# Performance work log

Measured on AMD Instinct MI355X. Metric: run time of the kernel, lower is better.

Reference implementation:

```python
import jax, jax.numpy as jnp
import numpy as np

B, L, F, P, E, H, D, C, V = 256, 100, 8, 4, 64, 4, 64, 32, 10000
HD = H * D  # 256 = att_dim * head_num
TOWER_IN = F * E + F * E + P * E + C  # 1312
LN_EPS = 1e-3  # keras LayerNormalization default epsilon


def _ln(x, g, b):
    m = jnp.mean(x, axis=-1, keepdims=True)
    v = jnp.mean(jnp.square(x - m), axis=-1, keepdims=True)
    return (x - m) * jax.lax.rsqrt(v + LN_EPS) * g + b


def setup_inputs() -> dict:
    key = jax.random.key(0)
    ks = jax.random.split(key, 32)
    w = lambda k, s: jax.random.normal(k, s, jnp.float32) * 0.02
    inp = {
        'target_ad': jax.random.randint(ks[0], (B, F), 0, V),
        'ubs_feature': jax.random.randint(ks[1], (B, L, F), 0, V),
        'profile_feature': jax.random.randint(ks[2], (B, P), 0, V),
        'context_feature': jax.random.normal(ks[3], (B, C), jnp.float32),
        # embedding tables: one per sparse feature, stacked
        'item_tables': w(ks[4], (F, V, E)),
        'profile_tables': w(ks[5], (P, V, E)),
        # per-timestep distinct attention weights, stacked over L
        'q_w': w(ks[6], (L, E, HD)),
        'k_w': w(ks[7], (L, E, HD)),
        'v_w': w(ks[8], (L, E, HD)),
        'lin_w': w(ks[9], (L, HD, E)),
        'lin_b': jnp.zeros((L, E), jnp.float32),
        # shared post-attention layernorm
        'ln_g': jnp.ones((E,), jnp.float32),
        'ln_b': jnp.zeros((E,), jnp.float32),
        # dense tower
        't_w1': w(ks[10], (TOWER_IN, 1024)), 't_b1': jnp.zeros((1024,), jnp.float32),
        't_g1': jnp.ones((1024,), jnp.float32), 't_bb1': jnp.zeros((1024,), jnp.float32),
        't_w2': w(ks[11], (1024, 512)), 't_b2': jnp.zeros((512,), jnp.float32),
        't_g2': jnp.ones((512,), jnp.float32), 't_bb2': jnp.zeros((512,), jnp.float32),
        't_w3': w(ks[12], (512, 256)), 't_b3': jnp.zeros((256,), jnp.float32),
        't_g3': jnp.ones((256,), jnp.float32), 't_bb3': jnp.zeros((256,), jnp.float32),
        't_w4': w(ks[13], (256, 1)), 't_b4': jnp.zeros((1,), jnp.float32),
    }
    return inp


def reference(target_ad, ubs_feature, profile_feature, context_feature,
              item_tables, profile_tables, q_w, k_w, v_w, lin_w, lin_b,
              ln_g, ln_b,
              t_w1, t_b1, t_g1, t_bb1,
              t_w2, t_b2, t_g2, t_bb2,
              t_w3, t_b3, t_g3, t_bb3,
              t_w4, t_b4):
    b = target_ad.shape[0]
    # embedding lookups (feature-wise tables)
    te = item_tables[jnp.arange(F)[None, :], target_ad]              # [B,F,E]
    ue = item_tables[jnp.arange(F)[None, None, :], ubs_feature]      # [B,L,F,E]
    pe = profile_tables[jnp.arange(P)[None, :], profile_feature]     # [B,P,E]

    # per-step distinct Q/K/V projections, batched over L via einsum
    q = jnp.einsum('blfe,leo->blfo', ue, q_w).reshape(b, L, F, H, D)
    k = jnp.einsum('blfe,leo->blfo', ue, k_w).reshape(b, L, F, H, D)
    v = jnp.einsum('blfe,leo->blfo', ue, v_w).reshape(b, L, F, H, D)
    scores = jnp.einsum('blfhd,blghd->blhfg', q, k) / jnp.sqrt(jnp.float32(D))
    attw = jax.nn.softmax(scores, axis=-1)                           # [B,L,H,F,F]
    att = jnp.einsum('blhfg,blghd->blfhd', attw, v).reshape(b, L, F, HD)
    att_out = jnp.einsum('blfo,loe->blfe', att, lin_w) + lin_b[None, :, None, :]
    # shared LayerNorm per step, summed over L (original accumulates into zeros_like)
    ubs_t = jnp.sum(_ln(att_out, ln_g, ln_b), axis=1)                # [B,F,E]
    ubs = jax.nn.relu(ubs_t / jnp.float32(L))

    total = jnp.concatenate([ubs.reshape(b, -1), te.reshape(b, -1),
                             pe.reshape(b, -1), context_feature], axis=-1)

    h = jax.nn.relu(_ln(total @ t_w1 + t_b1, t_g1, t_bb1))
    h = jax.nn.relu(_ln(h @ t_w2 + t_b2, t_g2, t_bb2))
    h = jax.nn.relu(_ln(h @ t_w3 + t_b3, t_g3, t_bb3))
    out = jax.nn.sigmoid(h @ t_w4 + t_b4)                            # [B,1]
    return out
```

## Files before the change

kernel.cpp:

```cpp
#include <hip/hip_runtime.h>
#include <hip/hip_bf16.h>

#define B_ 256
#define L_ 100
#define F_ 8
#define P_ 4
#define E_ 64
#define H_ 4
#define D_ 64
#define C_ 32
#define V_ 10000
#define TOWER_IN_ 1312
#define LN_EPS 0.001f
#define LCH_ 4
#define NCH_ 25
#define ZK_ 40

typedef __attribute__((ext_vector_type(8))) short bf8v;
typedef __attribute__((ext_vector_type(8))) unsigned short us8;
typedef __attribute__((ext_vector_type(4))) float f4v;

__device__ __forceinline__ unsigned short f2bf(float x) {
    __hip_bfloat16 h = __float2bfloat16(x);
    return __builtin_bit_cast(unsigned short, h);
}

#define BARRIER() do { \
    asm volatile("s_waitcnt lgkmcnt(0)" ::: "memory"); \
    __builtin_amdgcn_s_barrier(); \
    asm volatile("" ::: "memory"); \
} while (0)

__global__ __launch_bounds__(256) void prologue_kernel(
    const float* __restrict__ q_w, const float* __restrict__ k_w,
    const float* __restrict__ v_w, const float* __restrict__ lin_w,
    unsigned short* __restrict__ wsMT, unsigned short* __restrict__ wsWT,
    const float* __restrict__ w1, const float* __restrict__ w2,
    const float* __restrict__ w3,
    unsigned short* __restrict__ Wt1, unsigned short* __restrict__ Wt2,
    unsigned short* __restrict__ Wt3, float* __restrict__ ubs_acc)
{
    __shared__ float sA[64][68];
    __shared__ float sB[64][68];
    const int t = threadIdx.x;
    const int bx = blockIdx.x;

    if (bx < 400) {
        const int l = bx >> 2;
        const int h = bx & 3;
        const size_t obase = (size_t)(l * 4 + h) * 4096;
        const int te = t & 15, to = t >> 4;

        for (int i = 0; i < 16; ++i) {
            int idx = t + i * 256;
            int e = idx >> 6, d = idx & 63;
            sA[e][d] = q_w[(l * 64 + e) * 256 + h * 64 + d];
            sB[e][d] = k_w[(l * 64 + e) * 256 + h * 64 + d];
        }
        __syncthreads();
        {
            float acc[4][4];
            #pragma unroll
            for (int i = 0; i < 4; ++i)
                #pragma unroll
                for (int j = 0; j < 4; ++j) acc[i][j] = 0.f;
            for (int d0 = 0; d0 < 64; d0 += 4) {
                float4 a4[4], b4[4];
                #pragma unroll
                for (int i = 0; i < 4; ++i) a4[i] = *(const float4*)&sA[te + 16 * i][d0];
                #pragma unroll
                for (int j = 0; j < 4; ++j) b4[j] = *(const float4*)&sB[to + 16 * j][d0];
                #pragma unroll
                for (int i = 0; i < 4; ++i)
                    #pragma unroll
                    for (int j = 0; j < 4; ++j) {
                        acc[i][j] += a4[i].x * b4[j].x;
                        acc[i][j] += a4[i].y * b4[j].y;
                        acc[i][j] += a4[i].z * b4[j].z;
                        acc[i][j] += a4[i].w * b4[j].w;
                    }
            }
            #pragma unroll
            for (int j = 0; j < 4; ++j)
                #pragma unroll
                for (int i = 0; i < 4; ++i)
                    wsMT[obase + (to + 16 * j) * 64 + (te + 16 * i)] = f2bf(acc[i][j]);
        }
        __syncthreads();

        for (int i = 0; i < 16; ++i) {
            int idx = t + i * 256;
            int e = idx >> 6, d = idx & 63;
            sA[e][d] = v_w[(l * 64 + e) * 256 + h * 64 + d];
            int oo = idx & 63, dd = idx >> 6;
            sB[oo][dd] = lin_w[l * 16384 + (h * 64 + dd) * 64 + oo];
        }
        __syncthreads();
        {
            float acc[4][4];
            #pragma unroll
            for (int i = 0; i < 4; ++i)
                #pragma unroll
                for (int j = 0; j < 4; ++j) acc[i][j] = 0.f;
            for (int d0 = 0; d0 < 64; d0 += 4) {
                float4 a4[4], b4[4];
                #pragma unroll
                for (int i = 0; i < 4; ++i) a4[i] = *(const float4*)&sA[te + 16 * i][d0];
                #pragma unroll
                for (int j = 0; j < 4; ++j) b4[j] = *(const float4*)&sB[to + 16 * j][d0];
                #pragma unroll
                for (int i = 0; i < 4; ++i)
                    #pragma unroll
                    for (int j = 0; j < 4; ++j) {
                        acc[i][j] += a4[i].x * b4[j].x;
                        acc[i][j] += a4[i].y * b4[j].y;
                        acc[i][j] += a4[i].z * b4[j].z;
                        acc[i][j] += a4[i].w * b4[j].w;
                    }
            }
            #pragma unroll
            for (int j = 0; j < 4; ++j)
                #pragma unroll
                for (int i = 0; i < 4; ++i)
                    wsWT[obase + (to + 16 * j) * 64 + (te + 16 * i)] = f2bf(acc[i][j]);
        }
    } else if (bx < 2352) {
        float (*tile)[33] = (float (*)[33])sA;
        int bi = bx - 400;
        const float* src; unsigned short* dst; int K, N, tk, tn;
        if (bi < 1312)      { src = w1; dst = Wt1; K = 1312; N = 1024; tk = bi / 32;  tn = bi % 32; }
        else if (bi < 1824) { int i = bi - 1312; src = w2; dst = Wt2; K = 1024; N = 512; tk = i / 16; tn = i % 16; }
        else                { int i = bi - 1824; src = w3; dst = Wt3; K = 512;  N = 256; tk = i / 8;  tn = i % 8; }
        const int k0 = tk * 32, n0 = tn * 32;
        const int rr = t >> 5, cc = t & 31;
        #pragma unroll
        for (int i = 0; i < 4; ++i) {
            int r = rr * 4 + i;
            tile[r][cc] = src[(size_t)(k0 + r) * N + n0 + cc];
        }
        __syncthreads();
        #pragma unroll
        for (int i = 0; i < 4; ++i) {
            int r = rr * 4 + i;
            dst[(size_t)(n0 + r) * K + k0 + cc] = f2bf(tile[cc][r]);
        }
    } else {
        const int bi = bx - 2352;
        float4 z = {0.f, 0.f, 0.f, 0.f};
        *(float4*)(ubs_acc + (size_t)bi * 1024 + t * 4) = z;
    }
}

__global__ __launch_bounds__(256, 3) void attn_kernel(
    const int* __restrict__ ubs_feature, const float* __restrict__ item_tables,
    const unsigned short* __restrict__ wsMT, const unsigned short* __restrict__ wsWT,
    const float* __restrict__ lin_b, const float* __restrict__ ln_g,
    const float* __restrict__ ln_b, float* __restrict__ ubs_acc)
{
    __shared__ __align__(16) unsigned short sUE[64][72];
    __shared__ __align__(16) unsigned short sT[64][136];
    __shared__ __align__(16) unsigned short sZt[4][64][ZK_];
    __shared__ __align__(16) unsigned short sAblk[4][16][32];
    __shared__ float sLng[64], sLnb[64], sLinb[LCH_][64];

    const int t = threadIdx.x;
    const int c = blockIdx.x >> 5;
    const int b0 = (blockIdx.x & 31) * 8;
    const int wv = t >> 6, lane = t & 63, quad = lane >> 4, cl = lane & 15;
    const int role = wv >> 1, hlw = wv & 1;

    const int grow = wv * 16 + (lane >> 2);
    const int gseg = lane & 3;
    const int gb = b0 + (grow >> 3), gf = grow & 7;

    if (t < 64) { sLng[t] = ln_g[t]; sLnb[t] = ln_b[t]; }
    if (t >= 64 && t < 128) {
        #pragma unroll
        for (int li = 0; li < LCH_; ++li)
            sLinb[li][t - 64] = lin_b[(c * LCH_ + li) * 64 + (t - 64)];
    }

    int vidx[LCH_];
    #pragma unroll
    for (int li = 0; li < LCH_; ++li)
        vidx[li] = ubs_feature[(gb * L_ + c * LCH_ + li) * F_ + gf];

    float4 pf[4];
    bf8v bfrag[4][2];

    auto load_bfrag = [&](int lh) {
        const unsigned short* Bsrc = (role == 0 ? wsMT : wsWT) + ((size_t)lh * 4096);
        #pragma unroll
        for (int nt = 0; nt < 4; ++nt)
            #pragma unroll
            for (int k2 = 0; k2 < 2; ++k2)
                bfrag[nt][k2] = *(const bf8v*)(Bsrc + (nt * 16 + cl) * 64 + k2 * 32 + quad * 8);
    };
    auto load_pf = [&](int li) {
        const float* srcp = item_tables + ((size_t)gf * V_ + vidx[li]) * 64 + gseg * 16;
        #pragma unroll
        for (int j = 0; j < 4; ++j) pf[j] = ((const float4*)srcp)[j];
    };
    auto store_ue = [&]() {
        us8 u0, u1;
        u0[0] = f2bf(pf[0].x); u0[1] = f2bf(pf[0].y); u0[2] = f2bf(pf[0].z); u0[3] = f2bf(pf[0].w);
        u0[4] = f2bf(pf[1].x); u0[5] = f2bf(pf[1].y); u0[6] = f2bf(pf[1].z); u0[7] = f2bf(pf[1].w);
        u1[0] = f2bf(pf[2].x); u1[1] = f2bf(pf[2].y); u1[2] = f2bf(pf[2].z); u1[3] = f2bf(pf[2].w);
        u1[4] = f2bf(pf[3].x); u1[5] = f2bf(pf[3].y); u1[6] = f2bf(pf[3].z); u1[7] = f2bf(pf[3].w);
        *(us8*)&sUE[grow][gseg * 16]     = u0;
        *(us8*)&sUE[grow][gseg * 16 + 8] = u1;
    };

    load_pf(0);
    load_bfrag((c * LCH_) * 4 + hlw);
    store_ue();
    BARRIER();

    float lnacc[16];
    #pragma unroll
    for (int i = 0; i < 16; ++i) lnacc[i] = 0.f;

    for (int li = 0; li < LCH_; ++li) {
        const int l = c * LCH_ + li;

        if (li + 1 < LCH_) load_pf(li + 1);

        f4v accO[4];
        #pragma unroll
        for (int nt = 0; nt < 4; ++nt) accO[nt] = {0.f, 0.f, 0.f, 0.f};

        #pragma unroll
        for (int half = 0; half < 2; ++half) {
            #pragma unroll
            for (int m = 0; m < 4; ++m) {
                bf8v a0 = *(const bf8v*)&sUE[m * 16 + cl][quad * 8];
                bf8v a1 = *(const bf8v*)&sUE[m * 16 + cl][32 + quad * 8];
                #pragma unroll
                for (int nt = 0; nt < 4; ++nt) {
                    f4v acc = {0.f, 0.f, 0.f, 0.f};
                    acc = __builtin_amdgcn_mfma_f32_16x16x32_bf16(a0, bfrag[nt][0], acc, 0, 0, 0);
                    acc = __builtin_amdgcn_mfma_f32_16x16x32_bf16(a1, bfrag[nt][1], acc, 0, 0, 0);
                    if (role == 0) {
                        #pragma unroll
                        for (int j = 0; j < 4; ++j)
                            sT[m * 16 + quad * 4 + j][hlw * 64 + nt * 16 + cl] = f2bf(acc[j]);
                    } else {
                        ushort4 zp;
                        zp.x = f2bf(acc[0]); zp.y = f2bf(acc[1]);
                        zp.z = f2bf(acc[2]); zp.w = f2bf(acc[3]);
                        const int k0 = (quad >> 1) * 16 + hlw * 8 + (quad & 1) * 4;
                        *(ushort4*)&sZt[m][nt * 16 + cl][k0] = zp;
                    }
                }
            }
            if (half == 0)            load_bfrag(l * 4 + 2 + hlw);
            else if (li + 1 < LCH_)   load_bfrag((l + 1) * 4 + hlw);
            BARRIER();

            {
                const int p = wv;
                const bool valid = (cl >> 3) == (quad >> 1);
                #pragma unroll
                for (int hl = 0; hl < 2; ++hl) {
                    bf8v a0s = *(const bf8v*)&sT[p * 16 + cl][hl * 64 + quad * 8];
                    bf8v a1s = *(const bf8v*)&sT[p * 16 + cl][hl * 64 + 32 + quad * 8];
                    bf8v u0 = *(const bf8v*)&sUE[p * 16 + cl][quad * 8];
                    bf8v u1 = *(const bf8v*)&sUE[p * 16 + cl][32 + quad * 8];
                    f4v acc = {0.f, 0.f, 0.f, 0.f};
                    acc = __builtin_amdgcn_mfma_f32_16x16x32_bf16(a0s, u0, acc, 0, 0, 0);
                    acc = __builtin_amdgcn_mfma_f32_16x16x32_bf16(a1s, u1, acc, 0, 0, 0);
                    const int kk = hl * 8 + (cl & 7) + (cl >> 3) * 16;
                    #pragma unroll
                    for (int j = 0; j < 4; ++j) {
                        float v = acc[j] * 0.125f;
                        float mx = v;
                        mx = fmaxf(mx, __shfl_xor(mx, 1));
                        mx = fmaxf(mx, __shfl_xor(mx, 2));
                        mx = fmaxf(mx, __shfl_xor(mx, 4));
                        float ex = __expf(v - mx);
                        float sm = ex;
                        sm += __shfl_xor(sm, 1);
                        sm += __shfl_xor(sm, 2);
                        sm += __shfl_xor(sm, 4);
                        float aw = valid ? ex * __builtin_amdgcn_rcpf(sm) : 0.f;
                        sAblk[p][quad * 4 + j][kk] = f2bf(aw);
                    }
                }
            }

            {
                const int p = wv;
                bf8v a0p = *(const bf8v*)&sAblk[p][cl][quad * 8];
                #pragma unroll
                for (int nt = 0; nt < 4; ++nt) {
                    bf8v bz = *(const bf8v*)&sZt[p][nt * 16 + cl][quad * 8];
                    accO[nt] = __builtin_amdgcn_mfma_f32_16x16x32_bf16(a0p, bz, accO[nt], 0, 0, 0);
                }
            }
            BARRIER();
        }

        {
            float x[16];
            #pragma unroll
            for (int nt = 0; nt < 4; ++nt)
                #pragma unroll
                for (int j = 0; j < 4; ++j)
                    x[nt * 4 + j] = accO[nt][j] + sLinb[li][nt * 16 + cl];
            #pragma unroll
            for (int j = 0; j < 4; ++j) {
                float s = x[j] + x[4 + j] + x[8 + j] + x[12 + j];
                #pragma unroll
                for (int m = 1; m < 16; m <<= 1) s += __shfl_xor(s, m);
                float mean = s * (1.f / 64.f);
                float q = 0.f;
                #pragma unroll
                for (int nt = 0; nt < 4; ++nt) { float d = x[nt * 4 + j] - mean; q += d * d; }
                #pragma unroll
                for (int m = 1; m < 16; m <<= 1) q += __shfl_xor(q, m);
                float rst = rsqrtf(q * (1.f / 64.f) + LN_EPS);
                #pragma unroll
                for (int nt = 0; nt < 4; ++nt) {
                    int col = nt * 16 + cl;
                    lnacc[nt * 4 + j] += (x[nt * 4 + j] - mean) * rst * sLng[col] + sLnb[col];
                }
            }
        }

        if (li + 1 < LCH_) {
            store_ue();
            BARRIER();
        }
    }

    #pragma unroll
    for (int j = 0; j < 4; ++j) {
        const int row = wv * 16 + quad * 4 + j;
        const int b = b0 + (row >> 3), f = row & 7;
        #pragma unroll
        for (int nt = 0; nt < 4; ++nt)
            atomicAdd(&ubs_acc[(size_t)b * 512 + f * 64 + nt * 16 + cl], lnacc[nt * 4 + j]);
    }
}

__global__ __launch_bounds__(256) void reduceX_kernel(
    const float* __restrict__ ubs_acc,
    const int* __restrict__ target_ad, const int* __restrict__ profile_feature,
    const float* __restrict__ context,
    const float* __restrict__ item_tables, const float* __restrict__ profile_tables,
    unsigned short* __restrict__ X, float* __restrict__ statsAll)
{
    const int b = blockIdx.x, t = threadIdx.x;
    if (b == B_) {
        float4 z = {0.f, 0.f, 0.f, 0.f};
        ((float4*)statsAll)[t] = z;
        return;
    }
    const float2 v = *(const float2*)(ubs_acc + (size_t)b * 512 + t * 2);
    X[b * TOWER_IN_ + t * 2]     = f2bf(fmaxf(v.x * 0.01f, 0.f));
    X[b * TOWER_IN_ + t * 2 + 1] = f2bf(fmaxf(v.y * 0.01f, 0.f));
    for (int cc = 512 + t; cc < TOWER_IN_; cc += 256) {
        float x;
        if (cc < 1024) { int j = cc - 512, f = j >> 6, e = j & 63;
            x = item_tables[((size_t)f * V_ + target_ad[b * 8 + f]) * 64 + e]; }
        else if (cc < 1280) { int j = cc - 1024, pp = j >> 6, e = j & 63;
            x = profile_tables[((size_t)pp * V_ + profile_feature[b * 4 + pp]) * 64 + e]; }
        else x = context[b * 32 + (cc - 1280)];
        X[b * TOWER_IN_ + cc] = f2bf(x);
    }
}

__global__ __launch_bounds__(256) void gemm_kernel(
    const unsigned short* __restrict__ A, const unsigned short* __restrict__ Bw,
    const float* __restrict__ bias, float* __restrict__ C, int K, int N,
    float* __restrict__ stats)
{
    const int t = threadIdx.x;
    const int wv = t >> 6, lane = t & 63, quad = lane >> 4, cl = lane & 15;
    const int n0 = blockIdx.x * 64 + wv * 16;
    const int m0 = blockIdx.y * 16;
    f4v acc0 = {0.f, 0.f, 0.f, 0.f};
    f4v acc1 = {0.f, 0.f, 0.f, 0.f};
    const unsigned short* arow = A + (size_t)(m0 + cl) * K + quad * 8;
    const unsigned short* brow = Bw + (size_t)(n0 + cl) * K + quad * 8;
    int k0 = 0;
    #pragma unroll 2
    for (; k0 + 64 <= K; k0 += 64) {
        bf8v a0 = *(const bf8v*)(arow + k0);
        bf8v b0 = *(const bf8v*)(brow + k0);
        bf8v a1 = *(const bf8v*)(arow + k0 + 32);
        bf8v b1 = *(const bf8v*)(brow + k0 + 32);
        acc0 = __builtin_amdgcn_mfma_f32_16x16x32_bf16(a0, b0, acc0, 0, 0, 0);
        acc1 = __builtin_amdgcn_mfma_f32_16x16x32_bf16(a1, b1, acc1, 0, 0, 0);
    }
    if (k0 < K) {
        bf8v a = *(const bf8v*)(arow + k0);
        bf8v b = *(const bf8v*)(brow + k0);
        acc0 = __builtin_amdgcn_mfma_f32_16x16x32_bf16(a, b, acc0, 0, 0, 0);
    }
    float bv = bias[n0 + cl];
    float cj[4];
    #pragma unroll
    for (int j = 0; j < 4; ++j) {
        cj[j] = acc0[j] + acc1[j] + bv;
        C[(size_t)(m0 + quad * 4 + j) * N + n0 + cl] = cj[j];
    }
    if (stats) {
        #pragma unroll
        for (int j = 0; j < 4; ++j) {
            float s = cj[j], q = cj[j] * cj[j];
            #pragma unroll
            for (int m = 1; m < 16; m <<= 1) { s += __shfl_xor(s, m); q += __shfl_xor(q, m); }
            if (cl == 0) {
                const int row = m0 + quad * 4 + j;
                atomicAdd(&stats[row * 2], s);
                atomicAdd(&stats[row * 2 + 1], q);
            }
        }
    }
}

__global__ __launch_bounds__(256) void lnapply_kernel(
    const float* __restrict__ C, const float* __restrict__ stats,
    const float* __restrict__ g, const float* __restrict__ bb,
    unsigned short* __restrict__ Hx, int N, float invN)
{
    const int b = blockIdx.x, t = threadIdx.x;
    const float s = stats[b * 2], q = stats[b * 2 + 1];
    const float mean = s * invN;
    const float var  = q * invN - mean * mean;
    const float rst  = rsqrtf(fmaxf(var, 0.f) + LN_EPS);
    for (int j = t * 4; j < N; j += 1024) {
        float4 x = *(const float4*)(C + (size_t)b * N + j);
        ushort4 o;
        o.x = f2bf(fmaxf((x.x - mean) * rst * g[j]     + bb[j],     0.f));
        o.y = f2bf(fmaxf((x.y - mean) * rst * g[j + 1] + bb[j + 1], 0.f));
        o.z = f2bf(fmaxf((x.z - mean) * rst * g[j + 2] + bb[j + 2], 0.f));
        o.w = f2bf(fmaxf((x.w - mean) * rst * g[j + 3] + bb[j + 3], 0.f));
        *(ushort4*)(Hx + (size_t)b * N + j) = o;
    }
}

__device__ __forceinline__ float block_reduce_sum(float v, float* sRed) {
    #pragma unroll
    for (int m = 1; m < 64; m <<= 1) v += __shfl_xor(v, m, 64);
    int wave = threadIdx.x >> 6, lane = threadIdx.x & 63;
    __syncthreads();
    if (lane == 0) sRed[wave] = v;
    __syncthreads();
    return sRed[0] + sRed[1] + sRed[2] + sRed[3];
}

__global__ __launch_bounds__(256) void final_kernel(
    const float* __restrict__ C3, const float* __restrict__ g3,
    const float* __restrict__ bb3, const float* __restrict__ w4,
    const float* __restrict__ b4, float* __restrict__ out)
{
    __shared__ float sRed[4];
    const int b = blockIdx.x, t = threadIdx.x;
    float x = C3[b * 256 + t];
    float s = block_reduce_sum(x, sRed);
    float mean = s * (1.f / 256.f);
    float d = x - mean;
    __syncthreads();
    float q = block_reduce_sum(d * d, sRed);
    float rst = rsqrtf(q * (1.f / 256.f) + LN_EPS);
    float h = fmaxf(d * rst * g3[t] + bb3[t], 0.f);
    __syncthreads();
    float p = block_reduce_sum(h * w4[t], sRed);
    if (t == 0) out[b] = 1.f / (1.f + expf(-(p + b4[0])));
}

extern "C" void kernel_launch(void* const* d_in, const int* in_sizes, int n_in,
                              void* d_out, int out_size, void* d_ws, size_t ws_size,
                              hipStream_t stream)
{
    (void)in_sizes; (void)n_in; (void)out_size; (void)ws_size;
    const int*   target_ad       = (const int*)d_in[0];
    const int*   ubs_feature     = (const int*)d_in[1];
    const int*   profile_feature = (const int*)d_in[2];
    const float* context         = (const float*)d_in[3];
    const float* item_tables     = (const float*)d_in[4];
    const float* profile_tables  = (const float*)d_in[5];
    const float* q_w   = (const float*)d_in[6];
    const float* k_w   = (const float*)d_in[7];
    const float* v_w   = (const float*)d_in[8];
    const float* lin_w = (const float*)d_in[9];
    const float* lin_b = (const float*)d_in[10];
    const float* ln_g  = (const float*)d_in[11];
    const float* ln_b  = (const float*)d_in[12];
    const float* t_w1  = (const float*)d_in[13];
    const float* t_b1  = (const float*)d_in[14];
    const float* t_g1  = (const float*)d_in[15];
    const float* t_bb1 = (const float*)d_in[16];
    const float* t_w2  = (const float*)d_in[17];
    const float* t_b2  = (const float*)d_in[18];
    const float* t_g2  = (const float*)d_in[19];
    const float* t_bb2 = (const float*)d_in[20];
    const float* t_w3  = (const float*)d_in[21];
    const float* t_b3  = (const float*)d_in[22];
    const float* t_g3  = (const float*)d_in[23];
    const float* t_bb3 = (const float*)d_in[24];
    const float* t_w4  = (const float*)d_in[25];
    const float* t_b4  = (const float*)d_in[26];

    char* ws = (char*)d_ws;
    unsigned short* wsMT = (unsigned short*)(ws);
    unsigned short* wsWT = (unsigned short*)(ws +  3276800);
    float* ubs_acc       = (float*)         (ws +  6553600);
    unsigned short* Wt1  = (unsigned short*)(ws +  7077888);
    unsigned short* Wt2  = (unsigned short*)(ws +  9764864);
    unsigned short* Wt3  = (unsigned short*)(ws + 10813440);
    unsigned short* X    = (unsigned short*)(ws + 11075584);
    float*          C1   = (float*)         (ws + 11747328);
    unsigned short* H1   = (unsigned short*)(ws + 12795904);
    float*          C2   = (float*)         (ws + 13320192);
    unsigned short* H2   = (unsigned short*)(ws + 13844480);
    float*          C3   = (float*)         (ws + 14106624);
    float* stats1        = (float*)(ws);
    float* stats2        = (float*)(ws + 2048);

    prologue_kernel<<<2480, 256, 0, stream>>>(q_w, k_w, v_w, lin_w, wsMT, wsWT,
                                              t_w1, t_w2, t_w3, Wt1, Wt2, Wt3, ubs_acc);
    attn_kernel<<<NCH_ * 32, 256, 0, stream>>>(ubs_feature, item_tables, wsMT, wsWT,
                                               lin_b, ln_g, ln_b, ubs_acc);
    reduceX_kernel<<<B_ + 1, 256, 0, stream>>>(ubs_acc, target_ad, profile_feature, context,
                                               item_tables, profile_tables, X, stats1);
    gemm_kernel<<<dim3(16, 16), 256, 0, stream>>>(X,  Wt1, t_b1, C1, 1312, 1024, stats1);
    lnapply_kernel<<<B_, 256, 0, stream>>>(C1, stats1, t_g1, t_bb1, H1, 1024, 1.f / 1024.f);
    gemm_kernel<<<dim3(8, 16),  256, 0, stream>>>(H1, Wt2, t_b2, C2, 1024, 512, stats2);
    lnapply_kernel<<<B_, 256, 0, stream>>>(C2, stats2, t_g2, t_bb2, H2, 512, 1.f / 512.f);
    gemm_kernel<<<dim3(4, 16),  256, 0, stream>>>(H2, Wt3, t_b3, C3, 512, 256, (float*)nullptr);
    final_kernel<<<B_, 256, 0, stream>>>(C3, t_g3, t_bb3, t_w4, t_b4, (float*)d_out);
}
```

Measured before the change: 265.6 us.

## Fuse tower stages into fewer kernels and overlap weight transpose with attention

The tower weight transposes move from the prologue into the attention kernel launch as extra blocks, so they can run alongside attention work. The X-building step is fused into the first GEMM, and each LayerNorm+ReLU is fused into the next GEMM's A-tile load into LDS. The third GEMM is fused with the final LayerNorm, dot product and sigmoid. Together this cuts the launch count from nine to five and removes the intermediate X/H buffers and stats atomics, at the cost of recomputing per-row LN stats in every column block and using a smaller grid for the last GEMM.

Result: faster. 257.5 us (median of 2 runs) (-3.1%).

```diff
diff --git a/kernel.cpp b/kernel.cpp
--- a/kernel.cpp
+++ b/kernel.cpp
@@ -31,102 +31,125 @@
     asm volatile("" ::: "memory"); \
 } while (0)
 
-__global__ __launch_bounds__(256) void prologue_kernel(
+__global__ __launch_bounds__(256) void pre_kernel(
     const float* __restrict__ q_w, const float* __restrict__ k_w,
     const float* __restrict__ v_w, const float* __restrict__ lin_w,
     unsigned short* __restrict__ wsMT, unsigned short* __restrict__ wsWT,
-    const float* __restrict__ w1, const float* __restrict__ w2,
-    const float* __restrict__ w3,
-    unsigned short* __restrict__ Wt1, unsigned short* __restrict__ Wt2,
-    unsigned short* __restrict__ Wt3, float* __restrict__ ubs_acc)
+    float* __restrict__ ubs_acc)
 {
     __shared__ float sA[64][68];
     __shared__ float sB[64][68];
     const int t = threadIdx.x;
     const int bx = blockIdx.x;
 
-    if (bx < 400) {
-        const int l = bx >> 2;
-        const int h = bx & 3;
-        const size_t obase = (size_t)(l * 4 + h) * 4096;
-        const int te = t & 15, to = t >> 4;
-
-        for (int i = 0; i < 16; ++i) {
-            int idx = t + i * 256;
-            int e = idx >> 6, d = idx & 63;
-            sA[e][d] = q_w[(l * 64 + e) * 256 + h * 64 + d];
-            sB[e][d] = k_w[(l * 64 + e) * 256 + h * 64 + d];
-        }
-        __syncthreads();
-        {
-            float acc[4][4];
+    if (bx >= 400) {
+        const int bi = bx - 400;
+        float4 z = {0.f, 0.f, 0.f, 0.f};
+        *(float4*)(ubs_acc + (size_t)bi * 1024 + t * 4) = z;
+        return;
+    }
+
+    const int l = bx >> 2;
+    const int h = bx & 3;
+    const size_t obase = (size_t)(l * 4 + h) * 4096;
+    const int te = t & 15, to = t >> 4;
+
+    for (int i = 0; i < 16; ++i) {
+        int idx = t + i * 256;
+        int e = idx >> 6, d = idx & 63;
+        sA[e][d] = q_w[(l * 64 + e) * 256 + h * 64 + d];
+        sB[e][d] = k_w[(l * 64 + e) * 256 + h * 64 + d];
+    }
+    __syncthreads();
+    {
+        float acc[4][4];
+        #pragma unroll
+        for (int i = 0; i < 4; ++i)
+            #pragma unroll
+            for (int j = 0; j < 4; ++j) acc[i][j] = 0.f;
+        for (int d0 = 0; d0 < 64; d0 += 4) {
+            float4 a4[4], b4[4];
+            #pragma unroll
+            for (int i = 0; i < 4; ++i) a4[i] = *(const float4*)&sA[te + 16 * i][d0];
+            #pragma unroll
+            for (int j = 0; j < 4; ++j) b4[j] = *(const float4*)&sB[to + 16 * j][d0];
             #pragma unroll
             for (int i = 0; i < 4; ++i)
                 #pragma unroll
-                for (int j = 0; j < 4; ++j) acc[i][j] = 0.f;
-            for (int d0 = 0; d0 < 64; d0 += 4) {
-                float4 a4[4], b4[4];
-                #pragma unroll
-                for (int i = 0; i < 4; ++i) a4[i] = *(const float4*)&sA[te + 16 * i][d0];
-                #pragma unroll
-                for (int j = 0; j < 4; ++j) b4[j] = *(const float4*)&sB[to + 16 * j][d0];
-                #pragma unroll
-                for (int i = 0; i < 4; ++i)
-                    #pragma unroll
-                    for (int j = 0; j < 4; ++j) {
-                        acc[i][j] += a4[i].x * b4[j].x;
-                        acc[i][j] += a4[i].y * b4[j].y;
-                        acc[i][j] += a4[i].z * b4[j].z;
-                        acc[i][j] += a4[i].w * b4[j].w;
-                    }
-            }
-            #pragma unroll
-            for (int j = 0; j < 4; ++j)
-                #pragma unroll
-                for (int i = 0; i < 4; ++i)
-                    wsMT[obase + (to + 16 * j) * 64 + (te + 16 * i)] = f2bf(acc[i][j]);
-        }
-        __syncthreads();
-
-        for (int i = 0; i < 16; ++i) {
-            int idx = t + i * 256;
-            int e = idx >> 6, d = idx & 63;
-            sA[e][d] = v_w[(l * 64 + e) * 256 + h * 64 + d];
-            int oo = idx & 63, dd = idx >> 6;
-            sB[oo][dd] = lin_w[l * 16384 + (h * 64 + dd) * 64 + oo];
-        }
-        __syncthreads();
-        {
-            float acc[4][4];
+                for (int j = 0; j < 4; ++j) {
+                    acc[i][j] += a4[i].x * b4[j].x;
+                    acc[i][j] += a4[i].y * b4[j].y;
+                    acc[i][j] += a4[i].z * b4[j].z;
+                    acc[i][j] += a4[i].w * b4[j].w;
+                }
+        }
+        #pragma unroll
+        for (int j = 0; j < 4; ++j)
             #pragma unroll
             for (int i = 0; i < 4; ++i)
-                #pragma unroll
-                for (int j = 0; j < 4; ++j) acc[i][j] = 0.f;
-            for (int d0 = 0; d0 < 64; d0 += 4) {
-                float4 a4[4], b4[4];
-                #pragma unroll
-                for (int i = 0; i < 4; ++i) a4[i] = *(const float4*)&sA[te + 16 * i][d0];
-                #pragma unroll
-                for (int j = 0; j < 4; ++j) b4[j] = *(const float4*)&sB[to + 16 * j][d0];
-                #pragma unroll
-                for (int i = 0; i < 4; ++i)
-                    #pragma unroll
-                    for (int j = 0; j < 4; ++j) {
-                        acc[i][j] += a4[i].x * b4[j].x;
-                        acc[i][j] += a4[i].y * b4[j].y;
-                        acc[i][j] += a4[i].z * b4[j].z;
-                        acc[i][j] += a4[i].w * b4[j].w;
-                    }
-            }
-            #pragma unroll
-            for (int j = 0; j < 4; ++j)
-                #pragma unroll
-                for (int i = 0; i < 4; ++i)
-                    wsWT[obase + (to + 16 * j) * 64 + (te + 16 * i)] = f2bf(acc[i][j]);
-        }
-    } else if (bx < 2352) {
-        float (*tile)[33] = (float (*)[33])sA;
-        int bi = bx - 400;
+                wsMT[obase + (to + 16 * j) * 64 + (te + 16 * i)] = f2bf(acc[i][j]);
+    }
+    __syncthreads();
+
+    for (int i = 0; i < 16; ++i) {
+        int idx = t + i * 256;
+        int e = idx >> 6, d = idx & 63;
+        sA[e][d] = v_w[(l * 64 + e) * 256 + h * 64 + d];
+        int oo = idx & 63, dd = idx >> 6;
+        sB[oo][dd] = lin_w[l * 16384 + (h * 64 + dd) * 64 + oo];
+    }
+    __syncthreads();
+    {
+        float acc[4][4];
+        #pragma unroll
+        for (int i = 0; i < 4; ++i)
+            #pragma unroll
+            for (int j = 0; j < 4; ++j) acc[i][j] = 0.f;
+        for (int d0 = 0; d0 < 64; d0 += 4) {
+            float4 a4[4], b4[4];
+            #pragma unroll
+            for (int i = 0; i < 4; ++i) a4[i] = *(const float4*)&sA[te + 16 * i][d0];
+            #pragma unroll
+            for (int j = 0; j < 4; ++j) b4[j] = *(const float4*)&sB[to + 16 * j][d0];
+            #pragma unroll
+            for (int i = 0; i < 4; ++i)
+                #pragma unroll
+                for (int j = 0; j < 4; ++j) {
+                    acc[i][j] += a4[i].x * b4[j].x;
+                    acc[i][j] += a4[i].y * b4[j].y;
+                    acc[i][j] += a4[i].z * b4[j].z;
+                    acc[i][j] += a4[i].w * b4[j].w;
+                }
+        }
+        #pragma unroll
+        for (int j = 0; j < 4; ++j)
+            #pragma unroll
+            for (int i = 0; i < 4; ++i)
+                wsWT[obase + (to + 16 * j) * 64 + (te + 16 * i)] = f2bf(acc[i][j]);
+    }
+}
+
+__global__ __launch_bounds__(256, 3) void attn_kernel(
+    const int* __restrict__ ubs_feature, const float* __restrict__ item_tables,
+    const unsigned short* __restrict__ wsMT, const unsigned short* __restrict__ wsWT,
+    const float* __restrict__ lin_b, const float* __restrict__ ln_g,
+    const float* __restrict__ ln_b, float* __restrict__ ubs_acc,
+    const float* __restrict__ w1, const float* __restrict__ w2,
+    const float* __restrict__ w3,
+    unsigned short* __restrict__ Wt1, unsigned short* __restrict__ Wt2,
+    unsigned short* __restrict__ Wt3)
+{
+    __shared__ __align__(16) unsigned short sUE[64][72];
+    __shared__ __align__(16) unsigned short sT[64][136];
+    __shared__ __align__(16) unsigned short sZt[4][64][ZK_];
+    __shared__ __align__(16) unsigned short sAblk[4][16][32];
+    __shared__ float sLng[64], sLnb[64], sLinb[LCH_][64];
+
+    const int t = threadIdx.x;
+
+    if (blockIdx.x >= 800) {
+        float (*tile)[33] = (float (*)[33])sT;
+        int bi = blockIdx.x - 800;
         const float* src; unsigned short* dst; int K, N, tk, tn;
         if (bi < 1312)      { src = w1; dst = Wt1; K = 1312; N = 1024; tk = bi / 32;  tn = bi % 32; }
         else if (bi < 1824) { int i = bi - 1312; src = w2; dst = Wt2; K = 1024; N = 512; tk = i / 16; tn = i % 16; }
@@ -144,26 +167,9 @@
             int r = rr * 4 + i;
             dst[(size_t)(n0 + r) * K + k0 + cc] = f2bf(tile[cc][r]);
         }
-    } else {
-        const int bi = bx - 2352;
-        float4 z = {0.f, 0.f, 0.f, 0.f};
-        *(float4*)(ubs_acc + (size_t)bi * 1024 + t * 4) = z;
-    }
-}
-
-__global__ __launch_bounds__(256, 3) void attn_kernel(
-    const int* __restrict__ ubs_feature, const float* __restrict__ item_tables,
-    const unsigned short* __restrict__ wsMT, const unsigned short* __restrict__ wsWT,
-    const float* __restrict__ lin_b, const float* __restrict__ ln_g,
-    const float* __restrict__ ln_b, float* __restrict__ ubs_acc)
-{
-    __shared__ __align__(16) unsigned short sUE[64][72];
-    __shared__ __align__(16) unsigned short sT[64][136];
-    __shared__ __align__(16) unsigned short sZt[4][64][ZK_];
-    __shared__ __align__(16) unsigned short sAblk[4][16][32];
-    __shared__ float sLng[64], sLnb[64], sLinb[LCH_][64];
-
-    const int t = threadIdx.x;
+        return;
+    }
+
     const int c = blockIdx.x >> 5;
     const int b0 = (blockIdx.x & 31) * 8;
     const int wv = t >> 6, lane = t & 63, quad = lane >> 4, cl = lane & 15;
@@ -343,48 +349,17 @@
     }
 }
 
-__global__ __launch_bounds__(256) void reduceX_kernel(
-    const float* __restrict__ ubs_acc,
-    const int* __restrict__ target_ad, const int* __restrict__ profile_feature,
-    const float* __restrict__ context,
-    const float* __restrict__ item_tables, const float* __restrict__ profile_tables,
-    unsigned short* __restrict__ X, float* __restrict__ statsAll)
-{
-    const int b = blockIdx.x, t = threadIdx.x;
-    if (b == B_) {
-        float4 z = {0.f, 0.f, 0.f, 0.f};
-        ((float4*)statsAll)[t] = z;
-        return;
-    }
-    const float2 v = *(const float2*)(ubs_acc + (size_t)b * 512 + t * 2);
-    X[b * TOWER_IN_ + t * 2]     = f2bf(fmaxf(v.x * 0.01f, 0.f));
-    X[b * TOWER_IN_ + t * 2 + 1] = f2bf(fmaxf(v.y * 0.01f, 0.f));
-    for (int cc = 512 + t; cc < TOWER_IN_; cc += 256) {
-        float x;
-        if (cc < 1024) { int j = cc - 512, f = j >> 6, e = j & 63;
-            x = item_tables[((size_t)f * V_ + target_ad[b * 8 + f]) * 64 + e]; }
-        else if (cc < 1280) { int j = cc - 1024, pp = j >> 6, e = j & 63;
-            x = profile_tables[((size_t)pp * V_ + profile_feature[b * 4 + pp]) * 64 + e]; }
-        else x = context[b * 32 + (cc - 1280)];
-        X[b * TOWER_IN_ + cc] = f2bf(x);
-    }
-}
-
-__global__ __launch_bounds__(256) void gemm_kernel(
-    const unsigned short* __restrict__ A, const unsigned short* __restrict__ Bw,
-    const float* __restrict__ bias, float* __restrict__ C, int K, int N,
-    float* __restrict__ stats)
-{
-    const int t = threadIdx.x;
-    const int wv = t >> 6, lane = t & 63, quad = lane >> 4, cl = lane & 15;
-    const int n0 = blockIdx.x * 64 + wv * 16;
-    const int m0 = blockIdx.y * 16;
+__device__ __forceinline__ void gemm_from_lds(
+    const unsigned short* sA, int lda,
+    const unsigned short* __restrict__ Bw, const float* __restrict__ bias,
+    float* __restrict__ Cd, int K, int N, int n0w, int m0,
+    int quad, int cl)
+{
     f4v acc0 = {0.f, 0.f, 0.f, 0.f};
     f4v acc1 = {0.f, 0.f, 0.f, 0.f};
-    const unsigned short* arow = A + (size_t)(m0 + cl) * K + quad * 8;
-    const unsigned short* brow = Bw + (size_t)(n0 + cl) * K + quad * 8;
+    const unsigned short* arow = sA + cl * lda + quad * 8;
+    const unsigned short* brow = Bw + (size_t)(n0w + cl) * K + quad * 8;
     int k0 = 0;
-    #pragma unroll 2
     for (; k0 + 64 <= K; k0 += 64) {
         bf8v a0 = *(const bf8v*)(arow + k0);
         bf8v b0 = *(const bf8v*)(brow + k0);
@@ -398,77 +373,180 @@
         bf8v b = *(const bf8v*)(brow + k0);
         acc0 = __builtin_amdgcn_mfma_f32_16x16x32_bf16(a, b, acc0, 0, 0, 0);
     }
-    float bv = bias[n0 + cl];
-    float cj[4];
-    #pragma unroll
-    for (int j = 0; j < 4; ++j) {
-        cj[j] = acc0[j] + acc1[j] + bv;
-        C[(size_t)(m0 + quad * 4 + j) * N + n0 + cl] = cj[j];
-    }
-    if (stats) {
-        #pragma unroll
-        for (int j = 0; j < 4; ++j) {
-            float s = cj[j], q = cj[j] * cj[j];
-            #pragma unroll
-            for (int m = 1; m < 16; m <<= 1) { s += __shfl_xor(s, m); q += __shfl_xor(q, m); }
-            if (cl == 0) {
-                const int row = m0 + quad * 4 + j;
-                atomicAdd(&stats[row * 2], s);
-                atomicAdd(&stats[row * 2 + 1], q);
-            }
-        }
-    }
-}
-
-__global__ __launch_bounds__(256) void lnapply_kernel(
-    const float* __restrict__ C, const float* __restrict__ stats,
+    float bv = bias[n0w + cl];
+    #pragma unroll
+    for (int j = 0; j < 4; ++j)
+        Cd[(size_t)(m0 + quad * 4 + j) * N + n0w + cl] = acc0[j] + acc1[j] + bv;
+}
+
+__device__ __forceinline__ void ln_rows_to_lds(
+    const float* __restrict__ Cd, int N, int m0,
     const float* __restrict__ g, const float* __restrict__ bb,
-    unsigned short* __restrict__ Hx, int N, float invN)
-{
-    const int b = blockIdx.x, t = threadIdx.x;
-    const float s = stats[b * 2], q = stats[b * 2 + 1];
+    unsigned short* sH, int lda, int t, float invN)
+{
+    const int r = t >> 4, sub = t & 15;
+    const float* crow = Cd + (size_t)(m0 + r) * N;
+    float s = 0.f, s2 = 0.f;
+    for (int j = sub * 4; j < N; j += 64) {
+        float4 x = *(const float4*)(crow + j);
+        s  += x.x + x.y + x.z + x.w;
+        s2 += x.x * x.x + x.y * x.y + x.z * x.z + x.w * x.w;
+    }
+    #pragma unroll
+    for (int m = 1; m < 16; m <<= 1) { s += __shfl_xor(s, m); s2 += __shfl_xor(s2, m); }
     const float mean = s * invN;
-    const float var  = q * invN - mean * mean;
+    const float var  = s2 * invN - mean * mean;
     const float rst  = rsqrtf(fmaxf(var, 0.f) + LN_EPS);
-    for (int j = t * 4; j < N; j += 1024) {
-        float4 x = *(const float4*)(C + (size_t)b * N + j);
+    for (int j = sub * 4; j < N; j += 64) {
+        float4 x = *(const float4*)(crow + j);
         ushort4 o;
         o.x = f2bf(fmaxf((x.x - mean) * rst * g[j]     + bb[j],     0.f));
         o.y = f2bf(fmaxf((x.y - mean) * rst * g[j + 1] + bb[j + 1], 0.f));
         o.z = f2bf(fmaxf((x.z - mean) * rst * g[j + 2] + bb[j + 2], 0.f));
         o.w = f2bf(fmaxf((x.w - mean) * rst * g[j + 3] + bb[j + 3], 0.f));
-        *(ushort4*)(Hx + (size_t)b * N + j) = o;
-    }
-}
-
-__device__ __forceinline__ float block_reduce_sum(float v, float* sRed) {
-    #pragma unroll
-    for (int m = 1; m < 64; m <<= 1) v += __shfl_xor(v, m, 64);
-    int wave = threadIdx.x >> 6, lane = threadIdx.x & 63;
-    __syncthreads();
-    if (lane == 0) sRed[wave] = v;
-    __syncthreads();
-    return sRed[0] + sRed[1] + sRed[2] + sRed[3];
-}
-
-__global__ __launch_bounds__(256) void final_kernel(
-    const float* __restrict__ C3, const float* __restrict__ g3,
-    const float* __restrict__ bb3, const float* __restrict__ w4,
-    const float* __restrict__ b4, float* __restrict__ out)
-{
-    __shared__ float sRed[4];
-    const int b = blockIdx.x, t = threadIdx.x;
-    float x = C3[b * 256 + t];
-    float s = block_reduce_sum(x, sRed);
-    float mean = s * (1.f / 256.f);
-    float d = x - mean;
-    __syncthreads();
-    float q = block_reduce_sum(d * d, sRed);
-    float rst = rsqrtf(q * (1.f / 256.f) + LN_EPS);
-    float h = fmaxf(d * rst * g3[t] + bb3[t], 0.f);
-    __syncthreads();
-    float p = block_reduce_sum(h * w4[t], sRed);
-    if (t == 0) out[b] = 1.f / (1.f + expf(-(p + b4[0])));
+        *(ushort4*)&sH[r * lda + j] = o;
+    }
+}
+
+#define XLD 1320
+__global__ __launch_bounds__(256) void gemm1x_kernel(
+    const float* __restrict__ ubs_acc,
+    const int* __restrict__ target_ad, const int* __restrict__ profile_feature,
+    const float* __restrict__ context,
+    const float* __restrict__ item_tables, const float* __restrict__ profile_tables,
+    const unsigned short* __restrict__ Wt1, const float* __restrict__ b1,
+    float* __restrict__ C1)
+{
+    __shared__ __align__(16) unsigned short sX[16][XLD];
+    const int t = threadIdx.x;
+    const int wv = t >> 6, lane = t & 63, quad = lane >> 4, cl = lane & 15;
+    const int m0 = (blockIdx.x >> 4) * 16;
+    const int n0w = (blockIdx.x & 15) * 64 + wv * 16;
+
+    {
+        const int r = t >> 4, sub = t & 15;
+        const int gb = m0 + r;
+        #pragma unroll
+        for (int k = 0; k < 21; ++k) {
+            int cc = sub * 4 + k * 64;
+            if (cc >= TOWER_IN_) break;
+            float4 x;
+            if (cc < 512) {
+                x = *(const float4*)(ubs_acc + (size_t)gb * 512 + cc);
+                x.x = fmaxf(x.x * 0.01f, 0.f); x.y = fmaxf(x.y * 0.01f, 0.f);
+                x.z = fmaxf(x.z * 0.01f, 0.f); x.w = fmaxf(x.w * 0.01f, 0.f);
+            } else if (cc < 1024) {
+                int f = (cc - 512) >> 6, e = (cc - 512) & 63;
+                x = *(const float4*)(item_tables + ((size_t)f * V_ + target_ad[gb * 8 + f]) * 64 + e);
+            } else if (cc < 1280) {
+                int pp = (cc - 1024) >> 6, e = (cc - 1024) & 63;
+                x = *(const float4*)(profile_tables + ((size_t)pp * V_ + profile_feature[gb * 4 + pp]) * 64 + e);
+            } else {
+                x = *(const float4*)(context + (size_t)gb * 32 + (cc - 1280));
+            }
+            ushort4 o;
+            o.x = f2bf(x.x); o.y = f2bf(x.y); o.z = f2bf(x.z); o.w = f2bf(x.w);
+            *(ushort4*)&sX[r][cc] = o;
+        }
+    }
+    __syncthreads();
+    gemm_from_lds(&sX[0][0], XLD, Wt1, b1, C1, 1312, 1024, n0w, m0, quad, cl);
+}
+
+#define H1LD 1032
+__global__ __launch_bounds__(256) void gemm2f_kernel(
+    const float* __restrict__ C1, const float* __restrict__ g1,
+    const float* __restrict__ bb1,
+    const unsigned short* __restrict__ Wt2, const float* __restrict__ b2,
+    float* __restrict__ C2)
+{
+    __shared__ __align__(16) unsigned short sH[16][H1LD];
+    const int t = threadIdx.x;
+    const int wv = t >> 6, lane = t & 63, quad = lane >> 4, cl = lane & 15;
+    const int m0 = (blockIdx.x >> 3) * 16;
+    const int n0w = (blockIdx.x & 7) * 64 + wv * 16;
+
+    ln_rows_to_lds(C1, 1024, m0, g1, bb1, &sH[0][0], H1LD, t, 1.f / 1024.f);
+    __syncthreads();
+    gemm_from_lds(&sH[0][0], H1LD, Wt2, b2, C2, 1024, 512, n0w, m0, quad, cl);
+}
+
+#define H2LD 520
+__global__ __launch_bounds__(256) void gemm3f_kernel(
+    const float* __restrict__ C2, const float* __restrict__ g2,
+    const float* __restrict__ bb2,
+    const unsigned short* __restrict__ Wt3, const float* __restrict__ b3,
+    const float* __restrict__ g3, const float* __restrict__ bb3,
+    const float* __restrict__ w4, const float* __restrict__ b4,
+    float* __restrict__ out)
+{
+    __shared__ __align__(16) unsigned short sH[16][H2LD];
+    __shared__ float sS[4][16], sQ[4][16], sP[4][16];
+    const int t = threadIdx.x;
+    const int wv = t >> 6, lane = t & 63, quad = lane >> 4, cl = lane & 15;
+    const int m0 = blockIdx.x * 16;
+
+    ln_rows_to_lds(C2, 512, m0, g2, bb2, &sH[0][0], H2LD, t, 1.f / 512.f);
+    __syncthreads();
+
+    f4v acc[4];
+    #pragma unroll
+    for (int nt = 0; nt < 4; ++nt) acc[nt] = {0.f, 0.f, 0.f, 0.f};
+    for (int k0 = 0; k0 < 512; k0 += 32) {
+        bf8v a = *(const bf8v*)&sH[cl][k0 + quad * 8];
+        #pragma unroll
+        for (int nt = 0; nt < 4; ++nt) {
+            const int col0 = wv * 64 + nt * 16;
+            bf8v b = *(const bf8v*)(Wt3 + (size_t)(col0 + cl) * 512 + k0 + quad * 8);
+            acc[nt] = __builtin_amdgcn_mfma_f32_16x16x32_bf16(a, b, acc[nt], 0, 0, 0);
+        }
+    }
+    #pragma unroll
+    for (int nt = 0; nt < 4; ++nt) {
+        float bv = b3[wv * 64 + nt * 16 + cl];
+        #pragma unroll
+        for (int j = 0; j < 4; ++j) acc[nt][j] += bv;
+    }
+
+    #pragma unroll
+    for (int j = 0; j < 4; ++j) {
+        float s = acc[0][j] + acc[1][j] + acc[2][j] + acc[3][j];
+        float q = acc[0][j]*acc[0][j] + acc[1][j]*acc[1][j] + acc[2][j]*acc[2][j] + acc[3][j]*acc[3][j];
+        #pragma unroll
+        for (int m = 1; m < 16; m <<= 1) { s += __shfl_xor(s, m); q += __shfl_xor(q, m); }
+        if (cl == 0) { sS[wv][quad * 4 + j] = s; sQ[wv][quad * 4 + j] = q; }
+    }
+    __syncthreads();
+    float meanr[4], rstdr[4];
+    #pragma unroll
+    for (int j = 0; j < 4; ++j) {
+        const int row = quad * 4 + j;
+        float s = sS[0][row] + sS[1][row] + sS[2][row] + sS[3][row];
+        float q = sQ[0][row] + sQ[1][row] + sQ[2][row] + sQ[3][row];
+        float mean = s * (1.f / 256.f);
+        float var  = q * (1.f / 256.f) - mean * mean;
+        meanr[j] = mean;
+        rstdr[j] = rsqrtf(fmaxf(var, 0.f) + LN_EPS);
+    }
+
+    #pragma unroll
+    for (int j = 0; j < 4; ++j) {
+        float p = 0.f;
+        #pragma unroll
+        for (int nt = 0; nt < 4; ++nt) {
+            const int col = wv * 64 + nt * 16 + cl;
+            float h = fmaxf((acc[nt][j] - meanr[j]) * rstdr[j] * g3[col] + bb3[col], 0.f);
+            p += h * w4[col];
+        }
+        #pragma unroll
+        for (int m = 1; m < 16; m <<= 1) p += __shfl_xor(p, m);
+        if (cl == 0) sP[wv][quad * 4 + j] = p;
+    }
+    __syncthreads();
+    if (t < 16) {
+        float p = sP[0][t] + sP[1][t] + sP[2][t] + sP[3][t];
+        out[m0 + t] = 1.f / (1.f + expf(-(p + b4[0])));
+    }
 }
 
 extern "C" void kernel_launch(void* const* d_in, const int* in_sizes, int n_in,
@@ -511,25 +589,16 @@
     unsigned short* Wt1  = (unsigned short*)(ws +  7077888);
     unsigned short* Wt2  = (unsigned short*)(ws +  9764864);
     unsigned short* Wt3  = (unsigned short*)(ws + 10813440);
-    unsigned short* X    = (unsigned short*)(ws + 11075584);
-    float*          C1   = (float*)         (ws + 11747328);
-    unsigned short* H1   = (unsigned short*)(ws + 12795904);
-    float*          C2   = (float*)         (ws + 13320192);
-    unsigned short* H2   = (unsigned short*)(ws + 13844480);
-    float*          C3   = (float*)         (ws + 14106624);
-    float* stats1        = (float*)(ws);
-    float* stats2        = (float*)(ws + 2048);
-
-    prologue_kernel<<<2480, 256, 0, stream>>>(q_w, k_w, v_w, lin_w, wsMT, wsWT,
-                                              t_w1, t_w2, t_w3, Wt1, Wt2, Wt3, ubs_acc);
-    attn_kernel<<<NCH_ * 32, 256, 0, stream>>>(ubs_feature, item_tables, wsMT, wsWT,
-                                               lin_b, ln_g, ln_b, ubs_acc);
-    reduceX_kernel<<<B_ + 1, 256, 0, stream>>>(ubs_acc, target_ad, profile_feature, context,
-                                               item_tables, profile_tables, X, stats1);
-    gemm_kernel<<<dim3(16, 16), 256, 0, stream>>>(X,  Wt1, t_b1, C1, 1312, 1024, stats1);
-    lnapply_kernel<<<B_, 256, 0, stream>>>(C1, stats1, t_g1, t_bb1, H1, 1024, 1.f / 1024.f);
-    gemm_kernel<<<dim3(8, 16),  256, 0, stream>>>(H1, Wt2, t_b2, C2, 1024, 512, stats2);
-    lnapply_kernel<<<B_, 256, 0, stream>>>(C2, stats2, t_g2, t_bb2, H2, 512, 1.f / 512.f);
-    gemm_kernel<<<dim3(4, 16),  256, 0, stream>>>(H2, Wt3, t_b3, C3, 512, 256, (float*)nullptr);
-    final_kernel<<<B_, 256, 0, stream>>>(C3, t_g3, t_bb3, t_w4, t_b4, (float*)d_out);
-}
+    float*          C1   = (float*)         (ws + 11075584);
+    float*          C2   = (float*)         (ws + 12124160);
+
+    pre_kernel<<<528, 256, 0, stream>>>(q_w, k_w, v_w, lin_w, wsMT, wsWT, ubs_acc);
+    attn_kernel<<<800 + 1952, 256, 0, stream>>>(ubs_feature, item_tables, wsMT, wsWT,
+                                                lin_b, ln_g, ln_b, ubs_acc,
+                                                t_w1, t_w2, t_w3, Wt1, Wt2, Wt3);
+    gemm1x_kernel<<<256, 256, 0, stream>>>(ubs_acc, target_ad, profile_feature, context,
+                                           item_tables, profile_tables, Wt1, t_b1, C1);
+    gemm2f_kernel<<<128, 256, 0, stream>>>(C1, t_g1, t_bb1, Wt2, t_b2, C2);
+    gemm3f_kernel<<<16, 256, 0, stream>>>(C2, t_g2, t_bb2, Wt3, t_b3,
+                                          t_g3, t_bb3, t_w4, t_b4, (float*)d_out);
+}
```
